# Optimization experiments

Hardware: AMD Instinct MI355X
Metric: run time of the kernel (lower is better)

## Reference

```python
import jax, jax.numpy as jnp
import numpy as np

GRID_SIZE = 8
SPLINE_ORDER = 3
LAYERS = [256, 512, 512, 256]  # [input_dim] + hidden_dims
BATCH = 8192
BN_EPS = 1e-5


def make_grid(in_features):
    # efficient-kan/torchkan grid: uniform on [-1, 1] extended by spline_order on each side
    h = 2.0 / GRID_SIZE
    g = jnp.arange(-SPLINE_ORDER, GRID_SIZE + SPLINE_ORDER + 1, dtype=jnp.float32) * h - 1.0
    return jnp.broadcast_to(g, (in_features, g.shape[0]))  # (In, G + 2k + 1)


def b_splines(x, grid):
    # x: (B, In), grid: (In, G + 2k + 1) -> bases: (B, In, G + k)
    xg = x[:, :, None]
    bases = ((xg >= grid[:, :-1]) & (xg < grid[:, 1:])).astype(x.dtype)
    for k in range(1, SPLINE_ORDER + 1):
        left = (xg - grid[:, : -(k + 1)]) / (grid[:, k:-1] - grid[:, : -(k + 1)])
        right = (grid[:, k + 1 :] - xg) / (grid[:, k + 1 :] - grid[:, 1:-k])
        bases = left * bases[:, :, :-1] + right * bases[:, :, 1:]
    return bases


def kan_linear(x, grid, base_w, spline_w):
    # base path: GELU (exact, matching torch.nn.GELU) then linear
    base_out = jax.nn.gelu(x, approximate=False) @ base_w.T
    spline_out = jnp.einsum('bik,oik->bo', b_splines(x, grid), spline_w)
    return base_out + spline_out


def setup_inputs() -> dict:
    key = jax.random.key(0)
    ks = jax.random.split(key, 16)
    inp = {'x': jax.random.normal(ks[0], (BATCH, LAYERS[0]), dtype=jnp.float32)}
    n_bases = GRID_SIZE + SPLINE_ORDER
    for i, (fin, fout) in enumerate(zip(LAYERS[:-1], LAYERS[1:])):
        scale = 1.0 / np.sqrt(fin)
        inp[f'grid{i}'] = make_grid(fin)
        inp[f'base_w{i}'] = jax.random.normal(ks[1 + 3 * i], (fout, fin), dtype=jnp.float32) * scale
        inp[f'spline_w{i}'] = jax.random.normal(ks[2 + 3 * i], (fout, fin, n_bases), dtype=jnp.float32) * (0.1 * scale)
    d_out = LAYERS[-1]
    inp['bn_gamma'] = jnp.ones((d_out,), dtype=jnp.float32)
    inp['bn_beta'] = jnp.zeros((d_out,), dtype=jnp.float32)
    inp['bn_mean'] = jax.random.normal(ks[10], (d_out,), dtype=jnp.float32) * 0.1
    inp['bn_var'] = jax.random.uniform(ks[11], (d_out,), dtype=jnp.float32, minval=0.5, maxval=1.5)
    return inp


def reference(x, grid0, base_w0, spline_w0, grid1, base_w1, spline_w1, grid2, base_w2, spline_w2, bn_gamma, bn_beta, bn_mean, bn_var):
    h = kan_linear(x, grid0, base_w0, spline_w0)
    h = kan_linear(h, grid1, base_w1, spline_w1)
    h = kan_linear(h, grid2, base_w2, spline_w2)
    # BatchNorm1d in eval mode (running stats); Dropout is identity at inference
    return bn_gamma * (h - bn_mean) * jax.lax.rsqrt(bn_var + BN_EPS) + bn_beta
```

## Files before the change

kernel.cpp:

```cpp
#include <hip/hip_runtime.h>
#include <hip/hip_bf16.h>
#include <cstdint>


typedef unsigned short ushort_t;
typedef __bf16 bf16x8 __attribute__((ext_vector_type(8)));
typedef float f32x4 __attribute__((ext_vector_type(4)));

__device__ __forceinline__ ushort_t f2bf(float f) {
    __bf16 h = (__bf16)f;
    return __builtin_bit_cast(ushort_t, h);
}

__device__ __forceinline__ void gload_lds16(const void* g, void* lds) {
    __builtin_amdgcn_global_load_lds(
        (const __attribute__((address_space(1))) unsigned int*)(uintptr_t)g,
        (__attribute__((address_space(3))) unsigned int*)(unsigned int)(uintptr_t)lds,
        16, 0, 0);
}

__device__ __forceinline__ void expand12(float x, ushort_t* o) {
    float x3 = x * x * x;
    float y  = 0.7978845608028654f * (x + 0.044715f * x3);
    float e  = __expf(2.0f * y);
    float th = 1.0f - 2.0f / (e + 1.0f);
    o[0] = f2bf(0.5f * x * (1.0f + th));
    float xs = (x + 1.75f) * 4.0f;
#pragma unroll
    for (int j = 0; j < 11; ++j) {
        float t  = xs - (float)j;
        float a  = fabsf(t - 2.0f);
        float p1 = (3.0f * a - 6.0f) * a * a + 4.0f;
        float c  = 2.0f - a;
        float p2 = c * c * c;
        float v  = (a <= 1.0f) ? p1 : fmaxf(p2, 0.0f);
        o[1 + j] = f2bf(v * (1.0f / 6.0f));
    }
}

template <bool SUM>
__global__ __launch_bounds__(256) void expand_kernel(
    const float* __restrict__ X0, const float* __restrict__ X1,
    ushort_t* __restrict__ A, int total2)
{
    int idx = blockIdx.x * 256 + threadIdx.x;
    if (idx >= total2) return;
    float2 h = *(const float2*)(X0 + 2 * (size_t)idx);
    if (SUM) {
        float2 h2 = *(const float2*)(X1 + 2 * (size_t)idx);
        h.x += h2.x; h.y += h2.y;
    }
    union { ushort_t us[24]; uint4 v[3]; } pk;
    expand12(h.x, pk.us);
    expand12(h.y, pk.us + 12);
    uint4* dst = (uint4*)(A + (size_t)idx * 24);
    dst[0] = pk.v[0]; dst[1] = pk.v[1]; dst[2] = pk.v[2];
}

__global__ __launch_bounds__(256) void pack_w_kernel(
    const float* __restrict__ bw, const float* __restrict__ sw,
    ushort_t* __restrict__ W, int total)
{
    int idx = blockIdx.x * 256 + threadIdx.x;
    if (idx >= total) return;
    union { ushort_t us[12]; uint2 v[3]; } pk;
    pk.us[0] = f2bf(bw[idx]);
    const float* s = sw + (size_t)idx * 11;
#pragma unroll
    for (int k = 0; k < 11; ++k) pk.us[1 + k] = f2bf(s[k]);
    uint2* dst = (uint2*)(W + (size_t)idx * 12);
    dst[0] = pk.v[0]; dst[1] = pk.v[1]; dst[2] = pk.v[2];
}

#define SLOT 24576
#define ASZ  8192

__global__ __launch_bounds__(512, 2) void gemm_kernel(
    const ushort_t* __restrict__ A,
    const ushort_t* __restrict__ W,
    float* __restrict__ C,
    int M, int N, int K, int kcps)
{
    extern __shared__ __align__(16) ushort_t lds[];

    const int t   = threadIdx.x;
    const int l   = t & 63;
    const int wn  = (t >> 6) & 3;
    const int kg  = t >> 8;
    const int l15 = l & 15;
    const int q   = l >> 4;
    const int blockM = blockIdx.x * 128;
    const int blockN = blockIdx.y * 256;
    const int kb0 = blockIdx.z * kcps;
    const int nt  = kcps;
    float* Cz = C + (size_t)blockIdx.z * M * N;

    const ushort_t* Ab = A + (size_t)blockM * K;
    const ushort_t* Wb = W + (size_t)blockN * K;

    auto stage_a = [&](int kb, ushort_t* dst) {
#pragma unroll
        for (int it = 0; it < 2; ++it) {
            int s   = it * 512 + t;
            int row = s >> 3, c = s & 7;
            int g   = c ^ (row & 7);
            gload_lds16(Ab + ((size_t)row * K + (kb << 6) + g * 8), dst + s * 8);
        }
    };
    auto stage_b = [&](int kb, ushort_t* dst) {
#pragma unroll
        for (int it = 0; it < 4; ++it) {
            int s   = it * 512 + t;
            int row = s >> 3, c = s & 7;
            int g   = c ^ (row & 7);
            gload_lds16(Wb + ((size_t)row * K + (kb << 6) + g * 8), dst + s * 8);
        }
    };

    f32x4 acc[8][4];
#pragma unroll
    for (int i = 0; i < 8; ++i)
#pragma unroll
        for (int j = 0; j < 4; ++j) acc[i][j] = (f32x4){0.f, 0.f, 0.f, 0.f};

    stage_a(kb0, lds);            stage_b(kb0, lds + ASZ);
    stage_a(kb0 + 1, lds + SLOT); stage_b(kb0 + 1, lds + SLOT + ASZ);
    asm volatile("s_waitcnt vmcnt(6)" ::: "memory");
    __builtin_amdgcn_s_barrier();

    const int kc = kg * 4 + q;
    int cur = 0;
    for (int tt = 0; tt < nt; ++tt) {
        ushort_t* Ac = lds + cur * SLOT;
        ushort_t* Bc = Ac + ASZ;
        int nx = cur + 2; if (nx >= 3) nx -= 3;
        const bool pre = (tt + 2 < nt);

        if (pre) {
            ushort_t* An = lds + nx * SLOT;
            stage_a(kb0 + tt + 2, An);
            stage_b(kb0 + tt + 2, An + ASZ);
        }

        bf16x8 bfr[4], afr[8];
#pragma unroll
        for (int ni = 0; ni < 4; ++ni) {
            int n = wn * 64 + ni * 16 + l15;
            bfr[ni] = *(const bf16x8*)&Bc[(size_t)(n * 8 + (kc ^ (n & 7))) * 8];
        }
#pragma unroll
        for (int mi = 0; mi < 8; ++mi) {
            int m = mi * 16 + l15;
            afr[mi] = *(const bf16x8*)&Ac[(size_t)(m * 8 + (kc ^ (m & 7))) * 8];
        }
        __builtin_amdgcn_s_setprio(1);
#pragma unroll
        for (int mi = 0; mi < 8; ++mi)
#pragma unroll
            for (int ni = 0; ni < 4; ++ni)
                acc[mi][ni] = __builtin_amdgcn_mfma_f32_16x16x32_bf16(
                    afr[mi], bfr[ni], acc[mi][ni], 0, 0, 0);
        __builtin_amdgcn_s_setprio(0);

        asm volatile("s_waitcnt lgkmcnt(0)" ::: "memory");
        if (pre) asm volatile("s_waitcnt vmcnt(6)" ::: "memory");
        else     asm volatile("s_waitcnt vmcnt(0)" ::: "memory");
        __builtin_amdgcn_s_barrier();

        cur = cur + 1; if (cur == 3) cur = 0;
    }

    float* ldsf = (float*)lds;
    if (kg == 1) {
#pragma unroll
        for (int mi = 0; mi < 8; ++mi)
#pragma unroll
            for (int ni = 0; ni < 4; ++ni) {
                int col = wn * 64 + ni * 16 + l15;
#pragma unroll
                for (int r = 0; r < 4; ++r)
                    ldsf[(size_t)(mi * 16 + q * 4 + r) * 257 + col] = acc[mi][ni][r];
            }
    }
    __syncthreads();
    if (kg == 0) {
#pragma unroll
        for (int ni = 0; ni < 4; ++ni) {
            int col = wn * 64 + ni * 16 + l15;
            int n   = blockN + col;
#pragma unroll
            for (int mi = 0; mi < 8; ++mi) {
                int mb = blockM + mi * 16 + q * 4;
#pragma unroll
                for (int r = 0; r < 4; ++r) {
                    float v = acc[mi][ni][r] +
                              ldsf[(size_t)(mi * 16 + q * 4 + r) * 257 + col];
                    Cz[(size_t)(mb + r) * N + n] = v;
                }
            }
        }
    }
}

__global__ __launch_bounds__(256) void bn_reduce_kernel(
    const float4* __restrict__ Q0, const float4* __restrict__ Q1,
    const float4* __restrict__ Q2, const float4* __restrict__ Q3,
    const float* __restrict__ gamma, const float* __restrict__ beta,
    const float* __restrict__ mean,  const float* __restrict__ var,
    float4* __restrict__ out, int n4)
{
    int i = blockIdx.x * 256 + threadIdx.x;
    if (i >= n4) return;
    float4 a = Q0[i], b = Q1[i], c = Q2[i], d = Q3[i];
    int nb = (i * 4) & 255;
    float4 g  = *(const float4*)(gamma + nb);
    float4 be = *(const float4*)(beta + nb);
    float4 mn = *(const float4*)(mean + nb);
    float4 vr = *(const float4*)(var + nb);
    float4 o;
    o.x = g.x * rsqrtf(vr.x + 1e-5f) * (a.x + b.x + c.x + d.x - mn.x) + be.x;
    o.y = g.y * rsqrtf(vr.y + 1e-5f) * (a.y + b.y + c.y + d.y - mn.y) + be.y;
    o.z = g.z * rsqrtf(vr.z + 1e-5f) * (a.z + b.z + c.z + d.z - mn.z) + be.z;
    o.w = g.w * rsqrtf(vr.w + 1e-5f) * (a.w + b.w + c.w + d.w - mn.w) + be.w;
    out[i] = o;
}

extern "C" void kernel_launch(void* const* d_in, const int* in_sizes, int n_in,
                              void* d_out, int out_size, void* d_ws, size_t ws_size,
                              hipStream_t stream) {
    const float* x     = (const float*)d_in[0];
    const float* bw0   = (const float*)d_in[2];
    const float* sw0   = (const float*)d_in[3];
    const float* bw1   = (const float*)d_in[5];
    const float* sw1   = (const float*)d_in[6];
    const float* bw2   = (const float*)d_in[8];
    const float* sw2   = (const float*)d_in[9];
    const float* gamma = (const float*)d_in[10];
    const float* beta  = (const float*)d_in[11];
    const float* mean  = (const float*)d_in[12];
    const float* var   = (const float*)d_in[13];

    char* ws = (char*)d_ws;
    ushort_t* Abuf = (ushort_t*)(ws);
    ushort_t* W0   = (ushort_t*)(ws + 100663296);
    ushort_t* W1   = (ushort_t*)(ws + 103809024);
    ushort_t* W2   = (ushort_t*)(ws + 110100480);
    float*    P0   = (float*)(ws + 113246208);
    float*    P1   = (float*)(ws + 130023424);
    float*    Q0   = (float*)(ws + 113246208);
    float*    Q1   = (float*)(ws + 121634816);
    float*    Q2   = (float*)(ws + 130023424);
    float*    Q3   = (float*)(ws + 138412032);
    float*    out  = (float*)d_out;

    const size_t GEMM_LDS = 3 * SLOT * sizeof(ushort_t);

    pack_w_kernel<<<(512 * 256 + 255) / 256, 256, 0, stream>>>(bw0, sw0, W0, 512 * 256);
    pack_w_kernel<<<(512 * 512 + 255) / 256, 256, 0, stream>>>(bw1, sw1, W1, 512 * 512);
    pack_w_kernel<<<(256 * 512 + 255) / 256, 256, 0, stream>>>(bw2, sw2, W2, 256 * 512);

    expand_kernel<false><<<4096, 256, 0, stream>>>(x, nullptr, Abuf, 8192 * 256 / 2);
    {
        dim3 g(64, 2, 2);
        gemm_kernel<<<g, 512, GEMM_LDS, stream>>>(Abuf, W0, P0, 8192, 512, 3072, 24);
    }
    expand_kernel<true><<<8192, 256, 0, stream>>>(P0, P1, Abuf, 8192 * 512 / 2);
    {
        dim3 g(64, 2, 2);
        gemm_kernel<<<g, 512, GEMM_LDS, stream>>>(Abuf, W1, P0, 8192, 512, 6144, 48);
    }
    expand_kernel<true><<<8192, 256, 0, stream>>>(P0, P1, Abuf, 8192 * 512 / 2);
    {
        dim3 g(64, 1, 4);
        gemm_kernel<<<g, 512, GEMM_LDS, stream>>>(Abuf, W2, Q0, 8192, 256, 6144, 24);
    }
    bn_reduce_kernel<<<2048, 256, 0, stream>>>(
        (const float4*)Q0, (const float4*)Q1, (const float4*)Q2, (const float4*)Q3,
        gamma, beta, mean, var, (float4*)out, 8192 * 256 / 4);
}
```

Baseline: 297.3 us.

## Restructure GEMM to 256x256 tiles with K32 steps, 4-stage pipeline, fp16 split-K partials

The GEMM block tile changes from 128x256 with an intra-block K-split across two wave groups to 256x256 with waves split over M. That removes the LDS cross-wave reduction epilogue. The K step shrinks from 64 to 32, with a 4-slot pipeline prefetching three steps ahead and staged lgkmcnt waits interleaved with the MFMAs. Split-K across the grid grows to 4 or 8 slices, and the partials are stored as fp16 and summed in the expand and batch-norm kernels, cutting partial-buffer traffic. The risks are fp16 precision and range loss on partial sums, and more partial slices to read back.

```diff
diff --git a/kernel.cpp b/kernel.cpp
--- a/kernel.cpp
+++ b/kernel.cpp
@@ -6,6 +6,8 @@
 typedef unsigned short ushort_t;
 typedef __bf16 bf16x8 __attribute__((ext_vector_type(8)));
 typedef float f32x4 __attribute__((ext_vector_type(4)));
+typedef _Float16 f16x2 __attribute__((ext_vector_type(2)));
+typedef _Float16 f16x4 __attribute__((ext_vector_type(4)));
 
 __device__ __forceinline__ ushort_t f2bf(float f) {
     __bf16 h = (__bf16)f;
@@ -38,18 +40,12 @@
     }
 }
 
-template <bool SUM>
 __global__ __launch_bounds__(256) void expand_kernel(
-    const float* __restrict__ X0, const float* __restrict__ X1,
-    ushort_t* __restrict__ A, int total2)
+    const float* __restrict__ X0, ushort_t* __restrict__ A, int total2)
 {
     int idx = blockIdx.x * 256 + threadIdx.x;
     if (idx >= total2) return;
     float2 h = *(const float2*)(X0 + 2 * (size_t)idx);
-    if (SUM) {
-        float2 h2 = *(const float2*)(X1 + 2 * (size_t)idx);
-        h.x += h2.x; h.y += h2.y;
-    }
     union { ushort_t us[24]; uint4 v[3]; } pk;
     expand12(h.x, pk.us);
     expand12(h.y, pk.us + 12);
@@ -57,6 +53,25 @@
     dst[0] = pk.v[0]; dst[1] = pk.v[1]; dst[2] = pk.v[2];
 }
 
+__global__ __launch_bounds__(256) void expand_sum_kernel(
+    const _Float16* __restrict__ P, size_t pstride,
+    ushort_t* __restrict__ A, int total2)
+{
+    int idx = blockIdx.x * 256 + threadIdx.x;
+    if (idx >= total2) return;
+    float hx = 0.f, hy = 0.f;
+#pragma unroll
+    for (int s = 0; s < 4; ++s) {
+        f16x2 v = *(const f16x2*)(P + s * pstride + 2 * (size_t)idx);
+        hx += (float)v.x; hy += (float)v.y;
+    }
+    union { ushort_t us[24]; uint4 v[3]; } pk;
+    expand12(hx, pk.us);
+    expand12(hy, pk.us + 12);
+    uint4* dst = (uint4*)(A + (size_t)idx * 24);
+    dst[0] = pk.v[0]; dst[1] = pk.v[1]; dst[2] = pk.v[2];
+}
+
 __global__ __launch_bounds__(256) void pack_w_kernel(
     const float* __restrict__ bw, const float* __restrict__ sw,
     ushort_t* __restrict__ W, int total)
@@ -72,50 +87,48 @@
     dst[0] = pk.v[0]; dst[1] = pk.v[1]; dst[2] = pk.v[2];
 }
 
-#define SLOT 24576
-#define ASZ  8192
+#define SLOTE 16384
 
 __global__ __launch_bounds__(512, 2) void gemm_kernel(
     const ushort_t* __restrict__ A,
     const ushort_t* __restrict__ W,
-    float* __restrict__ C,
-    int M, int N, int K, int kcps)
+    _Float16* __restrict__ C,
+    int M, int N, int K, int scps)
 {
     extern __shared__ __align__(16) ushort_t lds[];
 
     const int t   = threadIdx.x;
     const int l   = t & 63;
-    const int wn  = (t >> 6) & 3;
-    const int kg  = t >> 8;
+    const int w   = t >> 6;
+    const int wm  = w >> 2;
+    const int wn  = w & 3;
     const int l15 = l & 15;
     const int q   = l >> 4;
-    const int blockM = blockIdx.x * 128;
+    const int blockM = blockIdx.x * 256;
     const int blockN = blockIdx.y * 256;
-    const int kb0 = blockIdx.z * kcps;
-    const int nt  = kcps;
-    float* Cz = C + (size_t)blockIdx.z * M * N;
+    const int kb0 = blockIdx.z * scps;
+    const int nt  = scps;
+    _Float16* Cz = C + (size_t)blockIdx.z * M * N;
 
     const ushort_t* Ab = A + (size_t)blockM * K;
     const ushort_t* Wb = W + (size_t)blockN * K;
 
-    auto stage_a = [&](int kb, ushort_t* dst) {
+    auto stage = [&](int kb, int slot) {
+        ushort_t* da = lds + slot * SLOTE;
+        ushort_t* db = da + 8192;
 #pragma unroll
         for (int it = 0; it < 2; ++it) {
-            int s   = it * 512 + t;
-            int row = s >> 3, c = s & 7;
-            int g   = c ^ (row & 7);
-            gload_lds16(Ab + ((size_t)row * K + (kb << 6) + g * 8), dst + s * 8);
+            int s = it * 512 + t;
+            int row = s >> 2, c = s & 3, g = c ^ (row & 3);
+            gload_lds16(Ab + ((size_t)row * K + (kb << 5) + g * 8), da + s * 8);
+        }
+#pragma unroll
+        for (int it = 0; it < 2; ++it) {
+            int s = it * 512 + t;
+            int row = s >> 2, c = s & 3, g = c ^ (row & 3);
+            gload_lds16(Wb + ((size_t)row * K + (kb << 5) + g * 8), db + s * 8);
         }
     };
-    auto stage_b = [&](int kb, ushort_t* dst) {
-#pragma unroll
-        for (int it = 0; it < 4; ++it) {
-            int s   = it * 512 + t;
-            int row = s >> 3, c = s & 7;
-            int g   = c ^ (row & 7);
-            gload_lds16(Wb + ((size_t)row * K + (kb << 6) + g * 8), dst + s * 8);
-        }
-    };
 
     f32x4 acc[8][4];
 #pragma unroll
@@ -123,105 +136,99 @@
 #pragma unroll
         for (int j = 0; j < 4; ++j) acc[i][j] = (f32x4){0.f, 0.f, 0.f, 0.f};
 
-    stage_a(kb0, lds);            stage_b(kb0, lds + ASZ);
-    stage_a(kb0 + 1, lds + SLOT); stage_b(kb0 + 1, lds + SLOT + ASZ);
-    asm volatile("s_waitcnt vmcnt(6)" ::: "memory");
+    stage(kb0 + 0, 0); stage(kb0 + 1, 1); stage(kb0 + 2, 2);
+    asm volatile("s_waitcnt vmcnt(8)" ::: "memory");
     __builtin_amdgcn_s_barrier();
 
-    const int kc = kg * 4 + q;
-    int cur = 0;
     for (int tt = 0; tt < nt; ++tt) {
-        ushort_t* Ac = lds + cur * SLOT;
-        ushort_t* Bc = Ac + ASZ;
-        int nx = cur + 2; if (nx >= 3) nx -= 3;
-        const bool pre = (tt + 2 < nt);
-
-        if (pre) {
-            ushort_t* An = lds + nx * SLOT;
-            stage_a(kb0 + tt + 2, An);
-            stage_b(kb0 + tt + 2, An + ASZ);
-        }
+        const int slot = tt & 3;
+        const ushort_t* Ac = lds + slot * SLOTE;
+        const ushort_t* Bc = Ac + 8192;
+
+        if (tt + 3 < nt) stage(kb0 + tt + 3, (tt + 3) & 3);
 
         bf16x8 bfr[4], afr[8];
 #pragma unroll
         for (int ni = 0; ni < 4; ++ni) {
             int n = wn * 64 + ni * 16 + l15;
-            bfr[ni] = *(const bf16x8*)&Bc[(size_t)(n * 8 + (kc ^ (n & 7))) * 8];
+            bfr[ni] = *(const bf16x8*)&Bc[(size_t)((n << 2) + (q ^ (n & 3))) * 8];
         }
 #pragma unroll
         for (int mi = 0; mi < 8; ++mi) {
-            int m = mi * 16 + l15;
-            afr[mi] = *(const bf16x8*)&Ac[(size_t)(m * 8 + (kc ^ (m & 7))) * 8];
-        }
+            int m = wm * 128 + mi * 16 + l15;
+            afr[mi] = *(const bf16x8*)&Ac[(size_t)((m << 2) + (q ^ (m & 3))) * 8];
+        }
+
+        asm volatile("s_waitcnt lgkmcnt(7)" ::: "memory");
+        __builtin_amdgcn_sched_barrier(0);
         __builtin_amdgcn_s_setprio(1);
 #pragma unroll
-        for (int mi = 0; mi < 8; ++mi)
+        for (int ni = 0; ni < 4; ++ni)
+            acc[0][ni] = __builtin_amdgcn_mfma_f32_16x16x32_bf16(
+                afr[0], bfr[ni], acc[0][ni], 0, 0, 0);
+
+        asm volatile("s_waitcnt lgkmcnt(4)" ::: "memory");
+        __builtin_amdgcn_sched_barrier(0);
+#pragma unroll
+        for (int mi = 1; mi < 4; ++mi)
+#pragma unroll
+            for (int ni = 0; ni < 4; ++ni)
+                acc[mi][ni] = __builtin_amdgcn_mfma_f32_16x16x32_bf16(
+                    afr[mi], bfr[ni], acc[mi][ni], 0, 0, 0);
+
+        asm volatile("s_waitcnt lgkmcnt(0)" ::: "memory");
+        __builtin_amdgcn_sched_barrier(0);
+#pragma unroll
+        for (int mi = 4; mi < 8; ++mi)
 #pragma unroll
             for (int ni = 0; ni < 4; ++ni)
                 acc[mi][ni] = __builtin_amdgcn_mfma_f32_16x16x32_bf16(
                     afr[mi], bfr[ni], acc[mi][ni], 0, 0, 0);
         __builtin_amdgcn_s_setprio(0);
 
-        asm volatile("s_waitcnt lgkmcnt(0)" ::: "memory");
-        if (pre) asm volatile("s_waitcnt vmcnt(6)" ::: "memory");
-        else     asm volatile("s_waitcnt vmcnt(0)" ::: "memory");
+        if (tt + 3 < nt)      asm volatile("s_waitcnt vmcnt(8)" ::: "memory");
+        else if (tt + 2 < nt) asm volatile("s_waitcnt vmcnt(4)" ::: "memory");
+        else if (tt + 1 < nt) asm volatile("s_waitcnt vmcnt(0)" ::: "memory");
         __builtin_amdgcn_s_barrier();
-
-        cur = cur + 1; if (cur == 3) cur = 0;
-    }
-
-    float* ldsf = (float*)lds;
-    if (kg == 1) {
-#pragma unroll
-        for (int mi = 0; mi < 8; ++mi)
-#pragma unroll
-            for (int ni = 0; ni < 4; ++ni) {
-                int col = wn * 64 + ni * 16 + l15;
-#pragma unroll
-                for (int r = 0; r < 4; ++r)
-                    ldsf[(size_t)(mi * 16 + q * 4 + r) * 257 + col] = acc[mi][ni][r];
-            }
-    }
-    __syncthreads();
-    if (kg == 0) {
-#pragma unroll
-        for (int ni = 0; ni < 4; ++ni) {
-            int col = wn * 64 + ni * 16 + l15;
-            int n   = blockN + col;
-#pragma unroll
-            for (int mi = 0; mi < 8; ++mi) {
-                int mb = blockM + mi * 16 + q * 4;
-#pragma unroll
-                for (int r = 0; r < 4; ++r) {
-                    float v = acc[mi][ni][r] +
-                              ldsf[(size_t)(mi * 16 + q * 4 + r) * 257 + col];
-                    Cz[(size_t)(mb + r) * N + n] = v;
-                }
-            }
+    }
+
+#pragma unroll
+    for (int ni = 0; ni < 4; ++ni) {
+        int n = blockN + wn * 64 + ni * 16 + l15;
+#pragma unroll
+        for (int mi = 0; mi < 8; ++mi) {
+            int mb = blockM + wm * 128 + mi * 16 + q * 4;
+#pragma unroll
+            for (int r = 0; r < 4; ++r)
+                Cz[(size_t)(mb + r) * N + n] = (_Float16)acc[mi][ni][r];
         }
     }
 }
 
 __global__ __launch_bounds__(256) void bn_reduce_kernel(
-    const float4* __restrict__ Q0, const float4* __restrict__ Q1,
-    const float4* __restrict__ Q2, const float4* __restrict__ Q3,
+    const _Float16* __restrict__ Q, size_t qstride,
     const float* __restrict__ gamma, const float* __restrict__ beta,
     const float* __restrict__ mean,  const float* __restrict__ var,
     float4* __restrict__ out, int n4)
 {
     int i = blockIdx.x * 256 + threadIdx.x;
     if (i >= n4) return;
-    float4 a = Q0[i], b = Q1[i], c = Q2[i], d = Q3[i];
+    float sx = 0.f, sy = 0.f, sz = 0.f, sw = 0.f;
+#pragma unroll
+    for (int s = 0; s < 8; ++s) {
+        f16x4 v = *(const f16x4*)(Q + s * qstride + 4 * (size_t)i);
+        sx += (float)v.x; sy += (float)v.y; sz += (float)v.z; sw += (float)v.w;
+    }
     int nb = (i * 4) & 255;
     float4 g  = *(const float4*)(gamma + nb);
     float4 be = *(const float4*)(beta + nb);
     float4 mn = *(const float4*)(mean + nb);
     float4 vr = *(const float4*)(var + nb);
     float4 o;
-    o.x = g.x * rsqrtf(vr.x + 1e-5f) * (a.x + b.x + c.x + d.x - mn.x) + be.x;
-    o.y = g.y * rsqrtf(vr.y + 1e-5f) * (a.y + b.y + c.y + d.y - mn.y) + be.y;
-    o.z = g.z * rsqrtf(vr.z + 1e-5f) * (a.z + b.z + c.z + d.z - mn.z) + be.z;
-    o.w = g.w * rsqrtf(vr.w + 1e-5f) * (a.w + b.w + c.w + d.w - mn.w) + be.w;
+    o.x = g.x * rsqrtf(vr.x + 1e-5f) * (sx - mn.x) + be.x;
+    o.y = g.y * rsqrtf(vr.y + 1e-5f) * (sy - mn.y) + be.y;
+    o.z = g.z * rsqrtf(vr.z + 1e-5f) * (sz - mn.z) + be.z;
+    o.w = g.w * rsqrtf(vr.w + 1e-5f) * (sw - mn.w) + be.w;
     out[i] = o;
 }
 
@@ -241,40 +248,36 @@
     const float* var   = (const float*)d_in[13];
 
     char* ws = (char*)d_ws;
-    ushort_t* Abuf = (ushort_t*)(ws);
-    ushort_t* W0   = (ushort_t*)(ws + 100663296);
-    ushort_t* W1   = (ushort_t*)(ws + 103809024);
-    ushort_t* W2   = (ushort_t*)(ws + 110100480);
-    float*    P0   = (float*)(ws + 113246208);
-    float*    P1   = (float*)(ws + 130023424);
-    float*    Q0   = (float*)(ws + 113246208);
-    float*    Q1   = (float*)(ws + 121634816);
-    float*    Q2   = (float*)(ws + 130023424);
-    float*    Q3   = (float*)(ws + 138412032);
-    float*    out  = (float*)d_out;
-
-    const size_t GEMM_LDS = 3 * SLOT * sizeof(ushort_t);
+    ushort_t*  Abuf = (ushort_t*)(ws);
+    ushort_t*  W0   = (ushort_t*)(ws + 100663296);
+    ushort_t*  W1   = (ushort_t*)(ws + 103809024);
+    ushort_t*  W2   = (ushort_t*)(ws + 110100480);
+    _Float16*  P    = (_Float16*)(ws + 113246208);
+    float*     out  = (float*)d_out;
+
+    const size_t PS01 = (size_t)8192 * 512;
+    const size_t PS2  = (size_t)8192 * 256;
+    const size_t GEMM_LDS = 4 * SLOTE * sizeof(ushort_t);
 
     pack_w_kernel<<<(512 * 256 + 255) / 256, 256, 0, stream>>>(bw0, sw0, W0, 512 * 256);
     pack_w_kernel<<<(512 * 512 + 255) / 256, 256, 0, stream>>>(bw1, sw1, W1, 512 * 512);
     pack_w_kernel<<<(256 * 512 + 255) / 256, 256, 0, stream>>>(bw2, sw2, W2, 256 * 512);
 
-    expand_kernel<false><<<4096, 256, 0, stream>>>(x, nullptr, Abuf, 8192 * 256 / 2);
+    expand_kernel<<<4096, 256, 0, stream>>>(x, Abuf, 8192 * 256 / 2);
     {
-        dim3 g(64, 2, 2);
-        gemm_kernel<<<g, 512, GEMM_LDS, stream>>>(Abuf, W0, P0, 8192, 512, 3072, 24);
-    }
-    expand_kernel<true><<<8192, 256, 0, stream>>>(P0, P1, Abuf, 8192 * 512 / 2);
+        dim3 g(32, 2, 4);
+        gemm_kernel<<<g, 512, GEMM_LDS, stream>>>(Abuf, W0, P, 8192, 512, 3072, 24);
+    }
+    expand_sum_kernel<<<8192, 256, 0, stream>>>(P, PS01, Abuf, 8192 * 512 / 2);
     {
-        dim3 g(64, 2, 2);
-        gemm_kernel<<<g, 512, GEMM_LDS, stream>>>(Abuf, W1, P0, 8192, 512, 6144, 48);
-    }
-    expand_kernel<true><<<8192, 256, 0, stream>>>(P0, P1, Abuf, 8192 * 512 / 2);
+        dim3 g(32, 2, 4);
+        gemm_kernel<<<g, 512, GEMM_LDS, stream>>>(Abuf, W1, P, 8192, 512, 6144, 48);
+    }
+    expand_sum_kernel<<<8192, 256, 0, stream>>>(P, PS01, Abuf, 8192 * 512 / 2);
     {
-        dim3 g(64, 1, 4);
-        gemm_kernel<<<g, 512, GEMM_LDS, stream>>>(Abuf, W2, Q0, 8192, 256, 6144, 24);
+        dim3 g(32, 1, 8);
+        gemm_kernel<<<g, 512, GEMM_LDS, stream>>>(Abuf, W2, P, 8192, 256, 6144, 24);
     }
     bn_reduce_kernel<<<2048, 256, 0, stream>>>(
-        (const float4*)Q0, (const float4*)Q1, (const float4*)Q2, (const float4*)Q3,
-        gamma, beta, mean, var, (float4*)out, 8192 * 256 / 4);
-}
+        P, PS2, gamma, beta, mean, var, (float4*)out, 8192 * 256 / 4);
+}
```

Measured after the change: 311.1 us. 1.05x slower.
